# Kernel optimization log

Hardware: AMD Instinct MI355X
Metric: run time of the kernel (lower is better)

## Reference

```python
import jax, jax.numpy as jnp
import numpy as np

STRIDES = (2, 2, 2)  # from init strides
BN_EPS = 1e-3        # keras BatchNormalization default epsilon


def upsample3d(x, s):
    # x: [B, D, H, W, C] -> nearest-neighbor repeat, like keras UpSampling3D
    x = jnp.repeat(x, s[0], axis=1)
    x = jnp.repeat(x, s[1], axis=2)
    return jnp.repeat(x, s[2], axis=3)


def _conv3d_same(xi, wi):
    # xi: [D, H, W, C]; wi: [kd, kh, kw, Cin, Cout] -> SAME, stride 1
    return jax.lax.conv_general_dilated(
        xi[None], wi, window_strides=(1, 1, 1), padding='SAME',
        dimension_numbers=('NDHWC', 'DHWIO', 'NDHWC'))[0]


# per-sample dynamic conv: each batch element uses its own hypernet kernel
per_sample_conv3d = jax.vmap(_conv3d_same, in_axes=(0, 0))


def batchnorm_train(x, gamma, beta):
    # training-mode BN over N,D,H,W axes
    mean = jnp.mean(x, axis=(0, 1, 2, 3), keepdims=True)
    var = jnp.var(x, axis=(0, 1, 2, 3), keepdims=True)
    return gamma * (x - mean) * jax.lax.rsqrt(var + BN_EPS) + beta


def setup_inputs() -> dict:
    key = jax.random.key(0)
    k1, k2, k3, k4 = jax.random.split(key, 4)
    B, D, H, W, Cin, Cmid = 4, 8, 32, 32, 128, 64
    x = jax.random.normal(k1, (B, D, H, W, Cin), dtype=jnp.float32)
    # scale kernels like fan-in init to keep activations sane
    w1 = jax.random.normal(k2, (B, 3, 3, 3, Cin, Cmid), dtype=jnp.float32) * 0.02
    w2 = jax.random.normal(k3, (B, 3, 3, 3, 2 * Cmid, Cmid), dtype=jnp.float32) * 0.02
    skip = jax.random.normal(k4, (B, 2 * D, 2 * H, 2 * W, Cmid), dtype=jnp.float32)
    return {
        'x': x, 'w1': w1, 'w2': w2, 'skip': skip,
        'gamma1': jnp.ones((Cmid,), jnp.float32),
        'beta1': jnp.zeros((Cmid,), jnp.float32),
        'gamma2': jnp.ones((Cmid,), jnp.float32),
        'beta2': jnp.zeros((Cmid,), jnp.float32),
        'training': 1,
    }


def reference(x, w1, w2, skip, gamma1, beta1, gamma2, beta2, training):
    x = upsample3d(x, STRIDES)                       # [B, 2D, 2H, 2W, Cin]
    x = per_sample_conv3d(x, w1)                     # [B, 2D, 2H, 2W, Cmid]
    x = batchnorm_train(x, gamma1, beta1)
    x = jax.nn.relu(x)
    x = jnp.concatenate([x, skip], axis=-1)          # [B, 2D, 2H, 2W, 2*Cmid]
    x = per_sample_conv3d(x, w2)                     # [B, 2D, 2H, 2W, Cmid]
    x = batchnorm_train(x, gamma2, beta2)
    return jax.nn.relu(x)
```

## Files before the change

kernel.cpp:

```cpp
#include <hip/hip_runtime.h>


typedef __attribute__((ext_vector_type(8))) short short8;
typedef __attribute__((ext_vector_type(4))) float f32x4;

__device__ __forceinline__ float bf2f(unsigned short u) {
  union { unsigned int i; float f; } v; v.i = ((unsigned int)u) << 16; return v.f;
}
__device__ __forceinline__ unsigned short f2b(float f) {
  union { float ff; unsigned int u; } v; v.ff = f;
  unsigned int x = v.u;
  return (unsigned short)((x + 0x7FFFu + ((x >> 16) & 1u)) >> 16);
}
__device__ __forceinline__ unsigned int pk2(float a, float b) {
  return (unsigned int)f2b(a) | ((unsigned int)f2b(b) << 16);
}
__device__ __forceinline__ void gload16(const void* g, void* l) {
  __builtin_amdgcn_global_load_lds(
      (const __attribute__((address_space(1))) void*)g,
      (__attribute__((address_space(3))) void*)l, 16, 0, 0);
}

#define ASTR 136
#define WSTR 132

__global__ __launch_bounds__(256) void hg_wt_k(const float* __restrict__ w1,
                                               const float* __restrict__ w2,
                                               unsigned short* __restrict__ wt1,
                                               unsigned short* __restrict__ wt2) {
  __shared__ short T[64 * ASTR];
  int blk = blockIdx.x;
  int sel = blk >= 108;
  const float* w = sel ? w2 : w1;
  unsigned short* wt = sel ? wt2 : wt1;
  int bt = sel ? blk - 108 : blk;
  const float* src = w + (size_t)bt * 8192;
  int tid = threadIdx.x;
  int co = tid & 63;
  int c0 = tid >> 6;
  for (int i = 0; i < 32; ++i) {
    int ci = c0 + (i << 2);
    T[co * ASTR + ci] = (short)f2b(src[(size_t)ci * 64 + co]);
  }
  __syncthreads();
  unsigned short* dst = wt + (size_t)bt * 8192;
  for (int i = 0; i < 4; ++i) {
    int task = tid + (i << 8);
    int row = task >> 4, q = task & 15;
    *(uint4*)(dst + row * 128 + (q << 3)) = *(const uint4*)&T[row * ASTR + (q << 3)];
  }
}

__global__ __launch_bounds__(256) void hg_wc1_k(const float* __restrict__ w1,
                                                unsigned short* __restrict__ wc1) {
  __shared__ short T[64 * ASTR];
  int blk = blockIdx.x;
  int b = blk >> 6, m = blk & 63;
  int dd = m >> 4, hh = (m >> 2) & 3, ww = m & 3;
  const int ks[4] = {0, 1, 0, 2}, kc[4] = {1, 2, 2, 1};
  int tid = threadIdx.x, co = tid & 63, c0 = tid >> 6;
  const float* wb = w1 + (size_t)b * 27 * 8192;
  for (int i = 0; i < 32; ++i) {
    int ci = c0 + (i << 2);
    float s = 0.f;
    for (int a = 0; a < kc[dd]; ++a)
      for (int e = 0; e < kc[hh]; ++e)
        for (int c = 0; c < kc[ww]; ++c) {
          int tap = ((ks[dd] + a) * 3 + ks[hh] + e) * 3 + ks[ww] + c;
          s += wb[(size_t)tap * 8192 + (size_t)ci * 64 + co];
        }
    T[co * ASTR + ci] = (short)f2b(s);
  }
  __syncthreads();
  unsigned short* dst = wc1 + (size_t)blk * 8192;
  for (int i = 0; i < 4; ++i) {
    int task = tid + (i << 8);
    int row = task >> 4, q = task & 15;
    *(uint4*)(dst + row * 128 + (q << 3)) = *(const uint4*)&T[row * ASTR + (q << 3)];
  }
}

__global__ __launch_bounds__(256, 3) void hg_c1p_k(
    const unsigned short* __restrict__ xb, const unsigned short* __restrict__ wc1,
    const unsigned short* __restrict__ zb, unsigned short* __restrict__ outb,
    float* __restrict__ sums) {
  __shared__ short Xl[2 * 100 * 128];
  int tid = threadIdx.x;
  int xcd = blockIdx.x & 7, slot = blockIdx.x >> 3;
  int b = xcd & 3;
  int t = ((xcd >> 2) << 7) + slot;
  int od = t >> 4, hti = (t >> 2) & 3, wti = t & 3;
  int pd = od & 1, md = od >> 1;
  int lane = tid & 63, quad = lane >> 4, l16 = lane & 15;
  int wid = tid >> 6;
  int ph = wid >> 1, pw = wid & 1;

  for (int pl = 0; pl < 2; ++pl) {
    int sd = md + pd - 1 + pl;
    int dok = ((unsigned)sd < 8u);
    for (int i = 0; i < 7; ++i) {
      int task = tid + (i << 8);
      if (task < 1600) {
        int pos = task >> 4, pq = task & 15;
        int q = (pq & 8) | ((pq & 7) ^ (pos & 7));
        int sh = pos / 10, sw = pos - sh * 10;
        int h = (hti << 3) + sh - 1, w = (wti << 3) + sw - 1;
        const unsigned short* src = zb;
        if (dok && (unsigned)h < 32u && (unsigned)w < 32u)
          src = xb + ((((size_t)(b * 8 + sd)) * 32 + h) * 32 + w) * 128 + (q << 3);
        gload16(src, (char*)Xl + ((pl * 1600 + (i << 8) + (tid & 192)) << 4));
      }
    }
  }
  __syncthreads();

  f32x4 acc[4][4];
#pragma unroll
  for (int i = 0; i < 4; ++i)
#pragma unroll
    for (int j = 0; j < 4; ++j) acc[i][j] = (f32x4){0.f, 0.f, 0.f, 0.f};

  const unsigned short* wcb = wc1 + ((size_t)b * 64 + (pd << 5) + (ph << 3) + (pw << 1)) * 8192;

  for (int td = 0; td < 2; ++td) {
    const char* Xp = (const char*)Xl + td * 25600;
    for (int th = 0; th < 2; ++th) {
      int hb = ph + th;
      for (int tw = 0; tw < 2; ++tw) {
        int wb2 = pw + tw;
        const unsigned short* wp = wcb + (size_t)((td << 4) + (th << 2) + tw) * 8192;
#pragma unroll
        for (int ksx = 0; ksx < 4; ++ksx) {
          int cq = (ksx << 2) + quad;
          short8 av[4], bv[4];
#pragma unroll
          for (int mt = 0; mt < 4; ++mt) {
            int pos = ((mt << 1) + (l16 >> 3) + hb) * 10 + (l16 & 7) + wb2;
            int pc = (cq & 8) | ((cq & 7) ^ (pos & 7));
            av[mt] = *(const short8*)(Xp + pos * 256 + (pc << 4));
          }
#pragma unroll
          for (int nt = 0; nt < 4; ++nt)
            bv[nt] = *(const short8*)(wp + ((nt << 4) + l16) * 128 + (cq << 3));
#pragma unroll
          for (int mt = 0; mt < 4; ++mt)
#pragma unroll
            for (int nt = 0; nt < 4; ++nt)
              acc[mt][nt] = __builtin_amdgcn_mfma_f32_16x16x32_bf16(
                  av[mt], bv[nt], acc[mt][nt], 0, 0, 0);
        }
      }
    }
  }

  __syncthreads();
  float* sbf = (float*)Xl;
  int rowb = (b * 16 + od) * 64;
#pragma unroll
  for (int nt = 0; nt < 4; ++nt) {
    int n = (nt << 4) + l16;
    float s = 0.f, q2 = 0.f;
#pragma unroll
    for (int mt = 0; mt < 4; ++mt) {
      int mh = (mt << 1) + (quad >> 1);
      int oh = (((hti << 3) + mh) << 1) + ph;
      size_t rb = (size_t)(rowb + oh) * 64;
#pragma unroll
      for (int r = 0; r < 4; ++r) {
        float v = acc[mt][nt][r];
        int ow = (((wti << 3) + ((quad & 1) << 2) + r) << 1) + pw;
        outb[(rb + ow) * 64 + n] = f2b(v);
        s += v; q2 += v * v;
      }
    }
    s += __shfl_xor(s, 16); s += __shfl_xor(s, 32);
    q2 += __shfl_xor(q2, 16); q2 += __shfl_xor(q2, 32);
    if (quad == 0) { sbf[wid * 128 + n] = s; sbf[wid * 128 + 64 + n] = q2; }
  }
  __syncthreads();
  if (tid < 64) {
    float s = sbf[tid] + sbf[128 + tid] + sbf[256 + tid] + sbf[384 + tid];
    float q2 = sbf[64 + tid] + sbf[192 + tid] + sbf[320 + tid] + sbf[448 + tid];
    atomicAdd(&sums[tid], s);
    atomicAdd(&sums[64 + tid], q2);
  }
}

__global__ __launch_bounds__(256) void hg_convf_k(
    const unsigned short* __restrict__ xb, const unsigned short* __restrict__ y1n,
    const unsigned short* __restrict__ skb, const unsigned short* __restrict__ wt,
    const unsigned short* __restrict__ zb,
    unsigned short* __restrict__ outb, float* __restrict__ outf,
    float* __restrict__ sums, int mode) {
  __shared__ short Al[132 * 128];
  __shared__ short Wl[64 * 128];
  int tid = threadIdx.x;
  int xcd = blockIdx.x & 7, slot = blockIdx.x >> 3;
  int b = xcd & 3;
  int t = ((xcd >> 2) << 8) + slot;
  int m0 = (b << 16) + (t << 7);
  int od  = (t >> 5) & 15;
  int oh0 = (t << 1) & 63;
  int lane = tid & 63, quad = lane >> 4, l16 = lane & 15;
  int wm = (tid >> 6) << 5;

  f32x4 acc[2][4];
  for (int i = 0; i < 2; ++i)
    for (int j = 0; j < 4; ++j) acc[i][j] = (f32x4){0.f, 0.f, 0.f, 0.f};

  const unsigned short* wb = wt + (size_t)b * 27 * 8192;

  for (int kd = 0; kd < 3; ++kd) {
    int ud = od + kd - 1;
    int dok = ((unsigned)ud < 16u);
    for (int kh = 0; kh < 3; ++kh) {
      __syncthreads();
      for (int i = 0; i < 9; ++i) {
        int task = tid + (i << 8);
        if (task < 2112) {
          int pos = task >> 4, pq = task & 15;
          int q = (pq & 8) | ((pq & 7) ^ (pos & 7));
          int g = (pos >= 66) ? 1 : 0;
          int uw = pos - (g ? 66 : 0) - 1;
          int uh = oh0 + g + kh - 1;
          const unsigned short* src = zb;
          if (dok && (unsigned)uh < 64u && (unsigned)uw < 64u) {
            if (mode == 0) {
              src = xb + ((((size_t)(b * 8 + (ud >> 1))) * 32 + (uh >> 1)) * 32 +
                          (uw >> 1)) * 128 + (q << 3);
            } else {
              size_t srow = (((size_t)(b * 16 + ud)) * 64 + uh) * 64 + uw;
              src = (q < 8) ? (y1n + srow * 64 + (q << 3))
                            : (skb + srow * 64 + ((q - 8) << 3));
            }
          }
          gload16(src, (char*)Al + (((i << 8) + (tid & 192)) << 4));
        }
      }
      for (int kw = 0; kw < 3; ++kw) {
        if (kw) __syncthreads();
        int tap = (kd * 3 + kh) * 3 + kw;
        const unsigned short* wsrc = wb + (size_t)tap * 8192;
        {
          int co0 = tid >> 4, pq = tid & 15;
          for (int i = 0; i < 4; ++i) {
            int co = co0 + (i << 4);
            int q = (pq & 8) | ((pq & 7) ^ (co & 7));
            gload16(wsrc + co * 128 + (q << 3),
                    (char*)Wl + (((i << 8) + (tid & 192)) << 4));
          }
        }
        __syncthreads();
        for (int k0 = 0; k0 < 128; k0 += 32) {
          int cq = (k0 >> 3) + quad;
          short8 av[2], bv[4];
          for (int mt = 0; mt < 2; ++mt) {
            int r = wm + (mt << 4) + l16;
            int pos = (r >> 6) * 66 + (r & 63) + kw;
            int pc = (cq & 8) | ((cq & 7) ^ (pos & 7));
            av[mt] = *(const short8*)((const char*)Al + pos * 256 + (pc << 4));
          }
          for (int nt = 0; nt < 4; ++nt) {
            int co = (nt << 4) + l16;
            int pc = (cq & 8) | ((cq & 7) ^ (co & 7));
            bv[nt] = *(const short8*)((const char*)Wl + co * 256 + (pc << 4));
          }
          for (int mt = 0; mt < 2; ++mt)
            for (int nt = 0; nt < 4; ++nt)
              acc[mt][nt] = __builtin_amdgcn_mfma_f32_16x16x32_bf16(
                  av[mt], bv[nt], acc[mt][nt], 0, 0, 0);
        }
      }
    }
  }

  __syncthreads();
  float* sbf = (float*)Al;
  for (int nt = 0; nt < 4; ++nt) {
    int n = (nt << 4) + l16;
    float s = 0.f, q2 = 0.f;
    for (int mt = 0; mt < 2; ++mt) {
      int mbase = m0 + wm + (mt << 4) + (quad << 2);
      for (int r = 0; r < 4; ++r) {
        float v = acc[mt][nt][r];
        size_t o = (size_t)(mbase + r) * 64 + n;
        if (mode == 0) outb[o] = f2b(v);
        else outf[o] = v;
        s += v; q2 += v * v;
      }
    }
    s += __shfl_xor(s, 16); s += __shfl_xor(s, 32);
    q2 += __shfl_xor(q2, 16); q2 += __shfl_xor(q2, 32);
    if (quad == 0) { sbf[(wm >> 5) * 128 + n] = s; sbf[(wm >> 5) * 128 + 64 + n] = q2; }
  }
  __syncthreads();
  if (tid < 64) {
    float s = sbf[tid] + sbf[128 + tid] + sbf[256 + tid] + sbf[384 + tid];
    float q2 = sbf[64 + tid] + sbf[192 + tid] + sbf[320 + tid] + sbf[448 + tid];
    atomicAdd(&sums[tid], s);
    atomicAdd(&sums[64 + tid], q2);
  }
}

__global__ __launch_bounds__(256) void hg_conv_o_k(
    const float* __restrict__ xf, const unsigned short* __restrict__ y1n,
    const float* __restrict__ skip, const float* __restrict__ wf,
    const unsigned short* __restrict__ wt, const float* __restrict__ bn,
    unsigned short* __restrict__ outb, float* __restrict__ outf,
    int mode, int has_wt) {
  __shared__ short Al[132 * ASTR];
  __shared__ short Wl[64 * WSTR];
  __shared__ float sbl[128];
  int tid = threadIdx.x;
  int xcd = blockIdx.x & 7, slot = blockIdx.x >> 3;
  int b = xcd & 3;
  int t = ((xcd >> 2) << 8) + slot;
  int m0 = (b << 16) + (t << 7);
  int od  = (t >> 5) & 15;
  int oh0 = (t << 1) & 63;
  int lane = tid & 63, quad = lane >> 4, l16 = lane & 15;
  int wm = (tid >> 6) << 5;

  if (mode == 1 && tid < 128) sbl[tid] = bn[tid];

  f32x4 acc[2][4];
  for (int i = 0; i < 2; ++i)
    for (int j = 0; j < 4; ++j) acc[i][j] = (f32x4){0.f, 0.f, 0.f, 0.f};

  const float* wbf = wf + (size_t)b * 27 * 8192;
  const unsigned short* wbt = wt + (size_t)b * 27 * 8192;

  for (int kd = 0; kd < 3; ++kd) {
    int ud = od + kd - 1;
    int dok = (ud >= 0 && ud < 16);
    for (int kh = 0; kh < 3; ++kh) {
      __syncthreads();
      for (int i = 0; i < 9; ++i) {
        int task = tid + (i << 8);
        if (task < 2112) {
          int chunk = task & 15;
          int pos = task >> 4;
          int g = (pos >= 66) ? 1 : 0;
          int uwi = pos - (g ? 66 : 0);
          int uh = oh0 + g + kh - 1;
          int uw = uwi - 1;
          uint4 val = make_uint4(0u, 0u, 0u, 0u);
          if (dok && (unsigned)uh < 64u && (unsigned)uw < 64u) {
            if (mode == 0) {
              size_t src = ((((size_t)(b * 8 + (ud >> 1))) * 32 + (uh >> 1)) * 32 +
                            (uw >> 1)) * 128 + (chunk << 3);
              float4 f0 = *(const float4*)(xf + src);
              float4 f1 = *(const float4*)(xf + src + 4);
              val.x = pk2(f0.x, f0.y); val.y = pk2(f0.z, f0.w);
              val.z = pk2(f1.x, f1.y); val.w = pk2(f1.z, f1.w);
            } else {
              size_t srow = (((size_t)(b * 16 + ud)) * 64 + uh) * 64 + uw;
              if (chunk < 8) {
                uint4 raw = *(const uint4*)(y1n + srow * 64 + (chunk << 3));
                unsigned int u[4] = {raw.x, raw.y, raw.z, raw.w};
                unsigned int o[4];
                int c0 = chunk << 3;
                for (int q = 0; q < 4; ++q) {
                  int c = c0 + q * 2;
                  float f0 = sbl[c] * bf2f((unsigned short)(u[q] & 0xFFFFu)) + sbl[64 + c];
                  float f1 = sbl[c + 1] * bf2f((unsigned short)(u[q] >> 16)) + sbl[64 + c + 1];
                  o[q] = pk2(f0 > 0.f ? f0 : 0.f, f1 > 0.f ? f1 : 0.f);
                }
                val = make_uint4(o[0], o[1], o[2], o[3]);
              } else {
                const float* sp = skip + srow * 64 + ((chunk - 8) << 3);
                float4 f0 = *(const float4*)(sp);
                float4 f1 = *(const float4*)(sp + 4);
                val.x = pk2(f0.x, f0.y); val.y = pk2(f0.z, f0.w);
                val.z = pk2(f1.x, f1.y); val.w = pk2(f1.z, f1.w);
              }
            }
          }
          *(uint4*)&Al[pos * ASTR + (chunk << 3)] = val;
        }
      }
      for (int kw = 0; kw < 3; ++kw) {
        if (kw) __syncthreads();
        int tap = (kd * 3 + kh) * 3 + kw;
        if (has_wt) {
          const unsigned short* wsrc = wbt + (size_t)tap * 8192;
          for (int i = 0; i < 4; ++i) {
            int task = tid + (i << 8);
            int co = task >> 4, q = task & 15;
            *(uint4*)&Wl[co * WSTR + (q << 3)] = *(const uint4*)(wsrc + co * 128 + (q << 3));
          }
        } else {
          const float* wp = wbf + (size_t)tap * 8192 + (tid & 63);
          int wco = tid & 63;
          int ci0 = (tid >> 6) << 5;
          for (int c = 0; c < 32; c += 2) {
            float f0 = wp[(size_t)(ci0 + c) * 64];
            float f1 = wp[(size_t)(ci0 + c + 1) * 64];
            *(unsigned int*)&Wl[wco * WSTR + ci0 + c] = pk2(f0, f1);
          }
        }
        __syncthreads();
        for (int k0 = 0; k0 < 128; k0 += 32) {
          int kk = k0 + (quad << 3);
          union { uint4 u; short8 s; } cv;
          short8 av[2];
          for (int mt = 0; mt < 2; ++mt) {
            int r = wm + (mt << 4) + l16;
            int g = r >> 6, ow = r & 63;
            cv.u = *(const uint4*)&Al[(g * 66 + ow + kw) * ASTR + kk];
            av[mt] = cv.s;
          }
          short8 bv[4];
          for (int nt = 0; nt < 4; ++nt) {
            int base = ((nt << 4) + l16) * WSTR + kk;
            uint2 lo = *(const uint2*)&Wl[base];
            uint2 hi = *(const uint2*)&Wl[base + 4];
            cv.u = make_uint4(lo.x, lo.y, hi.x, hi.y);
            bv[nt] = cv.s;
          }
          for (int mt = 0; mt < 2; ++mt)
            for (int nt = 0; nt < 4; ++nt)
              acc[mt][nt] = __builtin_amdgcn_mfma_f32_16x16x32_bf16(
                  av[mt], bv[nt], acc[mt][nt], 0, 0, 0);
        }
      }
    }
  }

  for (int mt = 0; mt < 2; ++mt) {
    int mbase = m0 + wm + (mt << 4) + (quad << 2);
    for (int nt = 0; nt < 4; ++nt) {
      int n = (nt << 4) + l16;
      for (int r = 0; r < 4; ++r) {
        float v = acc[mt][nt][r];
        size_t o = (size_t)(mbase + r) * 64 + n;
        if (mode == 0) outb[o] = f2b(v);
        else outf[o] = v;
      }
    }
  }
}

__global__ void hg_zero_k(float* __restrict__ p, int n) {
  for (int i = threadIdx.x; i < n; i += 256) p[i] = 0.f;
}

__global__ __launch_bounds__(256) void hg_stats_k(const unsigned short* __restrict__ yb,
                                                  const float* __restrict__ yf, int isf,
                                                  float* __restrict__ sums) {
  int t = threadIdx.x;
  int c = t & 63;
  int r0 = blockIdx.x * 4 + (t >> 6);
  float sum = 0.f, ss = 0.f;
  for (int r = r0; r < 262144; r += 4096) {
    size_t idx = (size_t)r * 64 + c;
    float v = isf ? yf[idx] : bf2f(yb[idx]);
    sum += v; ss += v * v;
  }
  atomicAdd(&sums[c], sum);
  atomicAdd(&sums[64 + c], ss);
}

__global__ void hg_fin_k(float* __restrict__ sb, const float* __restrict__ gm,
                         const float* __restrict__ bt) {
  int c = threadIdx.x;
  float invN = 1.f / 262144.f;
  float mean = sb[c] * invN;
  float var  = sb[64 + c] * invN - mean * mean;
  float sc = gm[c] * rsqrtf(var + 1e-3f);
  sb[c] = sc;
  sb[64 + c] = bt[c] - mean * sc;
}

__global__ __launch_bounds__(256) void hg_cvt_k(const float* __restrict__ s,
                                                unsigned short* __restrict__ d) {
  size_t i = ((size_t)blockIdx.x * 256 + threadIdx.x) << 3;
  float4 a = *(const float4*)(s + i);
  float4 c = *(const float4*)(s + i + 4);
  uint4 o;
  o.x = pk2(a.x, a.y); o.y = pk2(a.z, a.w);
  o.z = pk2(c.x, c.y); o.w = pk2(c.z, c.w);
  *(uint4*)(d + i) = o;
}

__global__ __launch_bounds__(256) void hg_bnb_k(unsigned short* __restrict__ y,
                                                const float* __restrict__ sb) {
  size_t i = ((size_t)blockIdx.x * 256 + threadIdx.x) << 3;
  int c0 = (int)(i & 63);
  uint4 v = *(uint4*)(y + i);
  unsigned int u[4] = {v.x, v.y, v.z, v.w};
  for (int q = 0; q < 4; ++q) {
    int c = c0 + q * 2;
    float f0 = sb[c] * bf2f((unsigned short)(u[q] & 0xFFFFu)) + sb[64 + c];
    float f1 = sb[c + 1] * bf2f((unsigned short)(u[q] >> 16)) + sb[64 + c + 1];
    u[q] = pk2(f0 > 0.f ? f0 : 0.f, f1 > 0.f ? f1 : 0.f);
  }
  *(uint4*)(y + i) = make_uint4(u[0], u[1], u[2], u[3]);
}

__global__ __launch_bounds__(256) void hg_bnrelu_f_k(float* __restrict__ y,
                                                     const float* __restrict__ sb) {
  size_t i = (size_t)blockIdx.x * 256 + threadIdx.x;
  int c4 = ((int)i & 15) << 2;
  float4 v = *(float4*)(y + i * 4);
  float f;
  f = sb[c4]     * v.x + sb[64 + c4];     v.x = f > 0.f ? f : 0.f;
  f = sb[c4 + 1] * v.y + sb[64 + c4 + 1]; v.y = f > 0.f ? f : 0.f;
  f = sb[c4 + 2] * v.z + sb[64 + c4 + 2]; v.z = f > 0.f ? f : 0.f;
  f = sb[c4 + 3] * v.w + sb[64 + c4 + 3]; v.w = f > 0.f ? f : 0.f;
  *(float4*)(y + i * 4) = v;
}

extern "C" void kernel_launch(void* const* d_in, const int* in_sizes, int n_in,
                              void* d_out, int out_size, void* d_ws, size_t ws_size,
                              hipStream_t stream) {
  (void)out_size;
  int ix = 0, iw1 = 1, iw2 = 2, isk = 3, ig1 = 4, ib1 = 5, ig2 = 6, ib2 = 7;
  if (n_in >= 9 && in_sizes[0] == 4194304 && in_sizes[1] == 884736 &&
      in_sizes[3] == 16777216 && in_sizes[4] == 64) {
  } else if (n_in >= 9 && in_sizes[0] == 64 && in_sizes[4] == 16777216 &&
             in_sizes[6] == 884736 && in_sizes[8] == 4194304) {
    ib1 = 0; ib2 = 1; ig1 = 2; ig2 = 3; isk = 4; iw1 = 6; iw2 = 7; ix = 8;
  } else {
    return;
  }
  if (ws_size < (32ull << 20) + 2048ull) return;

  const float* x    = (const float*)d_in[ix];
  const float* w1   = (const float*)d_in[iw1];
  const float* w2   = (const float*)d_in[iw2];
  const float* skip = (const float*)d_in[isk];
  const float* g1   = (const float*)d_in[ig1];
  const float* b1   = (const float*)d_in[ib1];
  const float* g2   = (const float*)d_in[ig2];
  const float* b2   = (const float*)d_in[ib2];
  float* out = (float*)d_out;

  const size_t OFF_SUMS = 32ull << 20;
  const size_t OFF_ZB   = OFF_SUMS + 2048;
  const size_t OFF_WT1  = OFF_ZB + 256;
  const size_t OFF_WT2  = OFF_WT1 + 1769472;
  const size_t OFF_XB   = OFF_WT2 + 1769472;
  const size_t OFF_SKB  = OFF_XB + 8388608;
  const size_t OFF_WC1  = OFF_SKB + 33554432;
  const size_t NEED     = OFF_WC1 + 4194304;

  unsigned short* y1 = (unsigned short*)d_ws;
  float* sums  = (float*)((char*)d_ws + OFF_SUMS);
  float* sums1 = sums;
  float* sums2 = sums + 128;

  if (ws_size >= NEED) {
    unsigned short* zb  = (unsigned short*)((char*)d_ws + OFF_ZB);
    unsigned short* wt1 = (unsigned short*)((char*)d_ws + OFF_WT1);
    unsigned short* wt2 = (unsigned short*)((char*)d_ws + OFF_WT2);
    unsigned short* xb  = (unsigned short*)((char*)d_ws + OFF_XB);
    unsigned short* skb = (unsigned short*)((char*)d_ws + OFF_SKB);
    unsigned short* wc1 = (unsigned short*)((char*)d_ws + OFF_WC1);

    hg_zero_k<<<1, 256, 0, stream>>>(sums, 576);
    hg_wt_k<<<216, 256, 0, stream>>>(w1, w2, wt1, wt2);
    hg_wc1_k<<<256, 256, 0, stream>>>(w1, wc1);
    hg_cvt_k<<<2048, 256, 0, stream>>>(x, xb);
    hg_cvt_k<<<8192, 256, 0, stream>>>(skip, skb);
    hg_c1p_k<<<1024, 256, 0, stream>>>(xb, wc1, zb, y1, sums1);
    hg_fin_k<<<1, 64, 0, stream>>>(sums1, g1, b1);
    hg_bnb_k<<<8192, 256, 0, stream>>>(y1, sums1);
    hg_convf_k<<<2048, 256, 0, stream>>>(xb, y1, skb, wt2, zb, y1, out, sums2, 1);
    hg_fin_k<<<1, 64, 0, stream>>>(sums2, g2, b2);
    hg_bnrelu_f_k<<<16384, 256, 0, stream>>>(out, sums2);
  } else {
    unsigned short* wt1 = (unsigned short*)((char*)d_ws + (32ull << 20) + 2048ull);
    unsigned short* wt2 = wt1 + 884736ull;
    const size_t WS_NEED = (32ull << 20) + 2048ull + 2ull * 884736ull * 2ull;
    int has_wt = (ws_size >= WS_NEED) ? 1 : 0;

    hg_zero_k<<<1, 256, 0, stream>>>(sums, 512);
    if (has_wt) hg_wt_k<<<216, 256, 0, stream>>>(w1, w2, wt1, wt2);
    hg_conv_o_k<<<2048, 256, 0, stream>>>(x, y1, skip, w1, wt1, sums1, y1, out, 0, has_wt);
    hg_stats_k<<<1024, 256, 0, stream>>>(y1, out, 0, sums1);
    hg_fin_k<<<1, 64, 0, stream>>>(sums1, g1, b1);
    hg_conv_o_k<<<2048, 256, 0, stream>>>(x, y1, skip, w2, wt2, sums1, y1, out, 1, has_wt);
    hg_stats_k<<<1024, 256, 0, stream>>>(y1, out, 1, sums2);
    hg_fin_k<<<1, 64, 0, stream>>>(sums2, g2, b2);
    hg_bnrelu_f_k<<<16384, 256, 0, stream>>>(out, sums2);
  }
}
```

Before: 462.6 us.

## Retile second conv into 128-thread 4x32 blocks and spread BN stat atomics

Replaces the generic second-conv kernel with a dedicated one. Each 128-thread block covers a 4-row by 32-column output tile and each wave holds a 4x4 MFMA accumulator set, which raises MFMA work per LDS weight load and reduces halo overhead per block. BatchNorm sum and sum-of-squares atomics are now split across 8 slots chosen by XCD, and a new finalize kernel adds them back together, to cut atomic contention on the same addresses. The risks are fewer waves per block, which may hurt latency hiding, and more registers per thread.

```diff
diff --git a/kernel.cpp b/kernel.cpp
--- a/kernel.cpp
+++ b/kernel.cpp
@@ -181,31 +181,31 @@
   if (tid < 64) {
     float s = sbf[tid] + sbf[128 + tid] + sbf[256 + tid] + sbf[384 + tid];
     float q2 = sbf[64 + tid] + sbf[192 + tid] + sbf[320 + tid] + sbf[448 + tid];
-    atomicAdd(&sums[tid], s);
-    atomicAdd(&sums[64 + tid], q2);
-  }
-}
-
-__global__ __launch_bounds__(256) void hg_convf_k(
-    const unsigned short* __restrict__ xb, const unsigned short* __restrict__ y1n,
-    const unsigned short* __restrict__ skb, const unsigned short* __restrict__ wt,
-    const unsigned short* __restrict__ zb,
-    unsigned short* __restrict__ outb, float* __restrict__ outf,
-    float* __restrict__ sums, int mode) {
-  __shared__ short Al[132 * 128];
+    int sl = (blockIdx.x & 7) << 7;
+    atomicAdd(&sums[sl + tid], s);
+    atomicAdd(&sums[sl + 64 + tid], q2);
+  }
+}
+
+__global__ __launch_bounds__(128) void hg_c2_k(
+    const unsigned short* __restrict__ y1n, const unsigned short* __restrict__ skb,
+    const unsigned short* __restrict__ wt, const unsigned short* __restrict__ zb,
+    float* __restrict__ outf, float* __restrict__ sums) {
+  __shared__ short Al[136 * 128];
   __shared__ short Wl[64 * 128];
   int tid = threadIdx.x;
   int xcd = blockIdx.x & 7, slot = blockIdx.x >> 3;
   int b = xcd & 3;
   int t = ((xcd >> 2) << 8) + slot;
-  int m0 = (b << 16) + (t << 7);
-  int od  = (t >> 5) & 15;
-  int oh0 = (t << 1) & 63;
+  int od = t >> 5, ohg = (t >> 1) & 15, owg = t & 1;
+  int oh0 = ohg << 2, ow0 = owg << 5;
   int lane = tid & 63, quad = lane >> 4, l16 = lane & 15;
-  int wm = (tid >> 6) << 5;
-
-  f32x4 acc[2][4];
-  for (int i = 0; i < 2; ++i)
+  int wid = tid >> 6;
+
+  f32x4 acc[4][4];
+#pragma unroll
+  for (int i = 0; i < 4; ++i)
+#pragma unroll
     for (int j = 0; j < 4; ++j) acc[i][j] = (f32x4){0.f, 0.f, 0.f, 0.f};
 
   const unsigned short* wb = wt + (size_t)b * 27 * 8192;
@@ -215,57 +215,54 @@
     int dok = ((unsigned)ud < 16u);
     for (int kh = 0; kh < 3; ++kh) {
       __syncthreads();
-      for (int i = 0; i < 9; ++i) {
-        int task = tid + (i << 8);
-        if (task < 2112) {
-          int pos = task >> 4, pq = task & 15;
-          int q = (pq & 8) | ((pq & 7) ^ (pos & 7));
-          int g = (pos >= 66) ? 1 : 0;
-          int uw = pos - (g ? 66 : 0) - 1;
-          int uh = oh0 + g + kh - 1;
-          const unsigned short* src = zb;
-          if (dok && (unsigned)uh < 64u && (unsigned)uw < 64u) {
-            if (mode == 0) {
-              src = xb + ((((size_t)(b * 8 + (ud >> 1))) * 32 + (uh >> 1)) * 32 +
-                          (uw >> 1)) * 128 + (q << 3);
-            } else {
-              size_t srow = (((size_t)(b * 16 + ud)) * 64 + uh) * 64 + uw;
-              src = (q < 8) ? (y1n + srow * 64 + (q << 3))
-                            : (skb + srow * 64 + ((q - 8) << 3));
-            }
-          }
-          gload16(src, (char*)Al + (((i << 8) + (tid & 192)) << 4));
-        }
+      for (int i = 0; i < 17; ++i) {
+        int task = tid + (i << 7);
+        int pos = task >> 4, pq = task & 15;
+        int q = (pq & 8) | ((pq & 7) ^ (pos & 7));
+        int g = pos / 34;
+        int uwi = pos - g * 34;
+        int uh = oh0 + g + kh - 1;
+        int uw = ow0 + uwi - 1;
+        const unsigned short* src = zb;
+        if (dok && (unsigned)uh < 64u && (unsigned)uw < 64u) {
+          size_t srow = (((size_t)(b * 16 + ud)) * 64 + uh) * 64 + uw;
+          src = (q < 8) ? (y1n + srow * 64 + (q << 3))
+                        : (skb + srow * 64 + ((q - 8) << 3));
+        }
+        gload16(src, (char*)Al + (((i << 7) + (tid & 64)) << 4));
       }
       for (int kw = 0; kw < 3; ++kw) {
         if (kw) __syncthreads();
         int tap = (kd * 3 + kh) * 3 + kw;
         const unsigned short* wsrc = wb + (size_t)tap * 8192;
-        {
-          int co0 = tid >> 4, pq = tid & 15;
-          for (int i = 0; i < 4; ++i) {
-            int co = co0 + (i << 4);
-            int q = (pq & 8) | ((pq & 7) ^ (co & 7));
-            gload16(wsrc + co * 128 + (q << 3),
-                    (char*)Wl + (((i << 8) + (tid & 192)) << 4));
-          }
+        for (int i = 0; i < 8; ++i) {
+          int task = tid + (i << 7);
+          int co = task >> 4, pq = task & 15;
+          int q = (pq & 8) | ((pq & 7) ^ (co & 7));
+          gload16(wsrc + co * 128 + (q << 3),
+                  (char*)Wl + (((i << 7) + (tid & 64)) << 4));
         }
         __syncthreads();
-        for (int k0 = 0; k0 < 128; k0 += 32) {
-          int cq = (k0 >> 3) + quad;
-          short8 av[2], bv[4];
-          for (int mt = 0; mt < 2; ++mt) {
-            int r = wm + (mt << 4) + l16;
-            int pos = (r >> 6) * 66 + (r & 63) + kw;
+#pragma unroll
+        for (int k0 = 0; k0 < 4; ++k0) {
+          int cq = (k0 << 2) + quad;
+          short8 av[4], bv[4];
+#pragma unroll
+          for (int mt = 0; mt < 4; ++mt) {
+            int mg = (wid << 2) + mt;
+            int pos = (mg >> 1) * 34 + ((mg & 1) << 4) + l16 + kw;
             int pc = (cq & 8) | ((cq & 7) ^ (pos & 7));
             av[mt] = *(const short8*)((const char*)Al + pos * 256 + (pc << 4));
           }
+#pragma unroll
           for (int nt = 0; nt < 4; ++nt) {
             int co = (nt << 4) + l16;
             int pc = (cq & 8) | ((cq & 7) ^ (co & 7));
             bv[nt] = *(const short8*)((const char*)Wl + co * 256 + (pc << 4));
           }
-          for (int mt = 0; mt < 2; ++mt)
+#pragma unroll
+          for (int mt = 0; mt < 4; ++mt)
+#pragma unroll
             for (int nt = 0; nt < 4; ++nt)
               acc[mt][nt] = __builtin_amdgcn_mfma_f32_16x16x32_bf16(
                   av[mt], bv[nt], acc[mt][nt], 0, 0, 0);
@@ -276,29 +273,35 @@
 
   __syncthreads();
   float* sbf = (float*)Al;
+  int rowb = (b * 16 + od) * 64;
+#pragma unroll
   for (int nt = 0; nt < 4; ++nt) {
     int n = (nt << 4) + l16;
     float s = 0.f, q2 = 0.f;
-    for (int mt = 0; mt < 2; ++mt) {
-      int mbase = m0 + wm + (mt << 4) + (quad << 2);
+#pragma unroll
+    for (int mt = 0; mt < 4; ++mt) {
+      int mg = (wid << 2) + mt;
+      int oh = oh0 + (mg >> 1);
+      int owb = ow0 + ((mg & 1) << 4) + (quad << 2);
+      size_t rb = ((size_t)(rowb + oh) * 64 + owb) * 64 + n;
+#pragma unroll
       for (int r = 0; r < 4; ++r) {
         float v = acc[mt][nt][r];
-        size_t o = (size_t)(mbase + r) * 64 + n;
-        if (mode == 0) outb[o] = f2b(v);
-        else outf[o] = v;
+        outf[rb + (size_t)r * 64] = v;
         s += v; q2 += v * v;
       }
     }
     s += __shfl_xor(s, 16); s += __shfl_xor(s, 32);
     q2 += __shfl_xor(q2, 16); q2 += __shfl_xor(q2, 32);
-    if (quad == 0) { sbf[(wm >> 5) * 128 + n] = s; sbf[(wm >> 5) * 128 + 64 + n] = q2; }
+    if (quad == 0) { sbf[wid * 128 + n] = s; sbf[wid * 128 + 64 + n] = q2; }
   }
   __syncthreads();
   if (tid < 64) {
-    float s = sbf[tid] + sbf[128 + tid] + sbf[256 + tid] + sbf[384 + tid];
-    float q2 = sbf[64 + tid] + sbf[192 + tid] + sbf[320 + tid] + sbf[448 + tid];
-    atomicAdd(&sums[tid], s);
-    atomicAdd(&sums[64 + tid], q2);
+    float s = sbf[tid] + sbf[128 + tid];
+    float q2 = sbf[64 + tid] + sbf[192 + tid];
+    int sl = (blockIdx.x & 7) << 7;
+    atomicAdd(&sums[sl + tid], s);
+    atomicAdd(&sums[sl + 64 + tid], q2);
   }
 }
 
@@ -472,6 +475,19 @@
   sb[64 + c] = bt[c] - mean * sc;
 }
 
+__global__ void hg_fin8_k(float* __restrict__ sb, const float* __restrict__ gm,
+                          const float* __restrict__ bt) {
+  int c = threadIdx.x;
+  float s = 0.f, q2 = 0.f;
+  for (int k = 0; k < 8; ++k) { s += sb[(k << 7) + c]; q2 += sb[(k << 7) + 64 + c]; }
+  float invN = 1.f / 262144.f;
+  float mean = s * invN;
+  float var  = q2 * invN - mean * mean;
+  float sc = gm[c] * rsqrtf(var + 1e-3f);
+  sb[c] = sc;
+  sb[64 + c] = bt[c] - mean * sc;
+}
+
 __global__ __launch_bounds__(256) void hg_cvt_k(const float* __restrict__ s,
                                                 unsigned short* __restrict__ d) {
   size_t i = ((size_t)blockIdx.x * 256 + threadIdx.x) << 3;
@@ -537,7 +553,7 @@
   float* out = (float*)d_out;
 
   const size_t OFF_SUMS = 32ull << 20;
-  const size_t OFF_ZB   = OFF_SUMS + 2048;
+  const size_t OFF_ZB   = OFF_SUMS + 8192;
   const size_t OFF_WT1  = OFF_ZB + 256;
   const size_t OFF_WT2  = OFF_WT1 + 1769472;
   const size_t OFF_XB   = OFF_WT2 + 1769472;
@@ -546,11 +562,11 @@
   const size_t NEED     = OFF_WC1 + 4194304;
 
   unsigned short* y1 = (unsigned short*)d_ws;
-  float* sums  = (float*)((char*)d_ws + OFF_SUMS);
-  float* sums1 = sums;
-  float* sums2 = sums + 128;
 
   if (ws_size >= NEED) {
+    float* sums  = (float*)((char*)d_ws + OFF_SUMS);
+    float* sums1 = sums;
+    float* sums2 = sums + 1024;
     unsigned short* zb  = (unsigned short*)((char*)d_ws + OFF_ZB);
     unsigned short* wt1 = (unsigned short*)((char*)d_ws + OFF_WT1);
     unsigned short* wt2 = (unsigned short*)((char*)d_ws + OFF_WT2);
@@ -558,18 +574,21 @@
     unsigned short* skb = (unsigned short*)((char*)d_ws + OFF_SKB);
     unsigned short* wc1 = (unsigned short*)((char*)d_ws + OFF_WC1);
 
-    hg_zero_k<<<1, 256, 0, stream>>>(sums, 576);
+    hg_zero_k<<<1, 256, 0, stream>>>(sums, 2112);
     hg_wt_k<<<216, 256, 0, stream>>>(w1, w2, wt1, wt2);
     hg_wc1_k<<<256, 256, 0, stream>>>(w1, wc1);
     hg_cvt_k<<<2048, 256, 0, stream>>>(x, xb);
     hg_cvt_k<<<8192, 256, 0, stream>>>(skip, skb);
     hg_c1p_k<<<1024, 256, 0, stream>>>(xb, wc1, zb, y1, sums1);
-    hg_fin_k<<<1, 64, 0, stream>>>(sums1, g1, b1);
+    hg_fin8_k<<<1, 64, 0, stream>>>(sums1, g1, b1);
     hg_bnb_k<<<8192, 256, 0, stream>>>(y1, sums1);
-    hg_convf_k<<<2048, 256, 0, stream>>>(xb, y1, skb, wt2, zb, y1, out, sums2, 1);
-    hg_fin_k<<<1, 64, 0, stream>>>(sums2, g2, b2);
+    hg_c2_k<<<2048, 128, 0, stream>>>(y1, skb, wt2, zb, out, sums2);
+    hg_fin8_k<<<1, 64, 0, stream>>>(sums2, g2, b2);
     hg_bnrelu_f_k<<<16384, 256, 0, stream>>>(out, sums2);
   } else {
+    float* sums  = (float*)((char*)d_ws + (32ull << 20));
+    float* sums1 = sums;
+    float* sums2 = sums + 128;
     unsigned short* wt1 = (unsigned short*)((char*)d_ws + (32ull << 20) + 2048ull);
     unsigned short* wt2 = wt1 + 884736ull;
     const size_t WS_NEED = (32ull << 20) + 2048ull + 2ull * 884736ull * 2ull;
```

After: 488.7 us. 5.6% more time.

## Read conv2 weights directly from global in fragment layout and shard BN stat atomics

Applied to the files above, without the earlier changes.

Adds a weight pre-pass that stores conv2 weights in an MFMA-fragment-friendly layout, so the conv2 kernel reads B operands straight from global/L2 instead of staging each tap through LDS. This removes the per-tap LDS weight copy and two barriers per tap, and adds a launch bound that asks for higher occupancy. BN statistic atomics are spread across 8 slots keyed by block index, and a new finalize kernel sums the slots, to cut atomic contention. The cost is more global/L2 traffic for weight fragments that are re-read by every wave.

```diff
diff --git a/kernel.cpp b/kernel.cpp
--- a/kernel.cpp
+++ b/kernel.cpp
@@ -48,6 +48,27 @@
     int task = tid + (i << 8);
     int row = task >> 4, q = task & 15;
     *(uint4*)(dst + row * 128 + (q << 3)) = *(const uint4*)&T[row * ASTR + (q << 3)];
+  }
+}
+
+__global__ __launch_bounds__(256) void hg_wtg_k(const float* __restrict__ w2,
+                                                unsigned short* __restrict__ wtg) {
+  __shared__ short T[64 * ASTR];
+  int bt = blockIdx.x;
+  const float* src = w2 + (size_t)bt * 8192;
+  int tid = threadIdx.x;
+  int co = tid & 63;
+  int c0 = tid >> 6;
+  for (int i = 0; i < 32; ++i) {
+    int ci = c0 + (i << 2);
+    T[co * ASTR + ci] = (short)f2b(src[(size_t)ci * 64 + co]);
+  }
+  __syncthreads();
+  unsigned short* dst = wtg + (size_t)bt * 8192;
+  for (int i = 0; i < 4; ++i) {
+    int task = tid + (i << 8);
+    int row = task >> 4, q = task & 15;
+    *(uint4*)(dst + ((q << 6) + row) * 8) = *(const uint4*)&T[row * ASTR + (q << 3)];
   }
 }
 
@@ -181,19 +202,17 @@
   if (tid < 64) {
     float s = sbf[tid] + sbf[128 + tid] + sbf[256 + tid] + sbf[384 + tid];
     float q2 = sbf[64 + tid] + sbf[192 + tid] + sbf[320 + tid] + sbf[448 + tid];
-    atomicAdd(&sums[tid], s);
-    atomicAdd(&sums[64 + tid], q2);
-  }
-}
-
-__global__ __launch_bounds__(256) void hg_convf_k(
-    const unsigned short* __restrict__ xb, const unsigned short* __restrict__ y1n,
-    const unsigned short* __restrict__ skb, const unsigned short* __restrict__ wt,
-    const unsigned short* __restrict__ zb,
-    unsigned short* __restrict__ outb, float* __restrict__ outf,
-    float* __restrict__ sums, int mode) {
+    int sl = (blockIdx.x & 7) << 7;
+    atomicAdd(&sums[sl + tid], s);
+    atomicAdd(&sums[sl + 64 + tid], q2);
+  }
+}
+
+__global__ __launch_bounds__(256, 4) void hg_c2g_k(
+    const unsigned short* __restrict__ y1n, const unsigned short* __restrict__ skb,
+    const unsigned short* __restrict__ wtg, const unsigned short* __restrict__ zb,
+    float* __restrict__ outf, float* __restrict__ sums) {
   __shared__ short Al[132 * 128];
-  __shared__ short Wl[64 * 128];
   int tid = threadIdx.x;
   int xcd = blockIdx.x & 7, slot = blockIdx.x >> 3;
   int b = xcd & 3;
@@ -208,7 +227,7 @@
   for (int i = 0; i < 2; ++i)
     for (int j = 0; j < 4; ++j) acc[i][j] = (f32x4){0.f, 0.f, 0.f, 0.f};
 
-  const unsigned short* wb = wt + (size_t)b * 27 * 8192;
+  const unsigned short* wb = wtg + (size_t)b * 27 * 8192;
 
   for (int kd = 0; kd < 3; ++kd) {
     int ud = od + kd - 1;
@@ -225,47 +244,34 @@
           int uh = oh0 + g + kh - 1;
           const unsigned short* src = zb;
           if (dok && (unsigned)uh < 64u && (unsigned)uw < 64u) {
-            if (mode == 0) {
-              src = xb + ((((size_t)(b * 8 + (ud >> 1))) * 32 + (uh >> 1)) * 32 +
-                          (uw >> 1)) * 128 + (q << 3);
-            } else {
-              size_t srow = (((size_t)(b * 16 + ud)) * 64 + uh) * 64 + uw;
-              src = (q < 8) ? (y1n + srow * 64 + (q << 3))
-                            : (skb + srow * 64 + ((q - 8) << 3));
-            }
+            size_t srow = (((size_t)(b * 16 + ud)) * 64 + uh) * 64 + uw;
+            src = (q < 8) ? (y1n + srow * 64 + (q << 3))
+                          : (skb + srow * 64 + ((q - 8) << 3));
           }
           gload16(src, (char*)Al + (((i << 8) + (tid & 192)) << 4));
         }
       }
+      __syncthreads();
+#pragma clang loop unroll(disable)
       for (int kw = 0; kw < 3; ++kw) {
-        if (kw) __syncthreads();
-        int tap = (kd * 3 + kh) * 3 + kw;
-        const unsigned short* wsrc = wb + (size_t)tap * 8192;
-        {
-          int co0 = tid >> 4, pq = tid & 15;
-          for (int i = 0; i < 4; ++i) {
-            int co = co0 + (i << 4);
-            int q = (pq & 8) | ((pq & 7) ^ (co & 7));
-            gload16(wsrc + co * 128 + (q << 3),
-                    (char*)Wl + (((i << 8) + (tid & 192)) << 4));
-          }
-        }
-        __syncthreads();
-        for (int k0 = 0; k0 < 128; k0 += 32) {
-          int cq = (k0 >> 3) + quad;
+        const unsigned short* wp = wb + (size_t)((kd * 3 + kh) * 3 + kw) * 8192;
+#pragma unroll
+        for (int k0 = 0; k0 < 4; ++k0) {
+          int cq = (k0 << 2) + quad;
           short8 av[2], bv[4];
+#pragma unroll
           for (int mt = 0; mt < 2; ++mt) {
             int r = wm + (mt << 4) + l16;
             int pos = (r >> 6) * 66 + (r & 63) + kw;
             int pc = (cq & 8) | ((cq & 7) ^ (pos & 7));
             av[mt] = *(const short8*)((const char*)Al + pos * 256 + (pc << 4));
           }
-          for (int nt = 0; nt < 4; ++nt) {
-            int co = (nt << 4) + l16;
-            int pc = (cq & 8) | ((cq & 7) ^ (co & 7));
-            bv[nt] = *(const short8*)((const char*)Wl + co * 256 + (pc << 4));
-          }
+#pragma unroll
+          for (int nt = 0; nt < 4; ++nt)
+            bv[nt] = *(const short8*)(wp + (((cq << 6) + (nt << 4) + l16) << 3));
+#pragma unroll
           for (int mt = 0; mt < 2; ++mt)
+#pragma unroll
             for (int nt = 0; nt < 4; ++nt)
               acc[mt][nt] = __builtin_amdgcn_mfma_f32_16x16x32_bf16(
                   av[mt], bv[nt], acc[mt][nt], 0, 0, 0);
@@ -283,9 +289,7 @@
       int mbase = m0 + wm + (mt << 4) + (quad << 2);
       for (int r = 0; r < 4; ++r) {
         float v = acc[mt][nt][r];
-        size_t o = (size_t)(mbase + r) * 64 + n;
-        if (mode == 0) outb[o] = f2b(v);
-        else outf[o] = v;
+        outf[(size_t)(mbase + r) * 64 + n] = v;
         s += v; q2 += v * v;
       }
     }
@@ -297,8 +301,9 @@
   if (tid < 64) {
     float s = sbf[tid] + sbf[128 + tid] + sbf[256 + tid] + sbf[384 + tid];
     float q2 = sbf[64 + tid] + sbf[192 + tid] + sbf[320 + tid] + sbf[448 + tid];
-    atomicAdd(&sums[tid], s);
-    atomicAdd(&sums[64 + tid], q2);
+    int sl = (blockIdx.x & 7) << 7;
+    atomicAdd(&sums[sl + tid], s);
+    atomicAdd(&sums[sl + 64 + tid], q2);
   }
 }
 
@@ -472,6 +477,19 @@
   sb[64 + c] = bt[c] - mean * sc;
 }
 
+__global__ void hg_fin8_k(float* __restrict__ sb, const float* __restrict__ gm,
+                          const float* __restrict__ bt) {
+  int c = threadIdx.x;
+  float s = 0.f, q2 = 0.f;
+  for (int k = 0; k < 8; ++k) { s += sb[(k << 7) + c]; q2 += sb[(k << 7) + 64 + c]; }
+  float invN = 1.f / 262144.f;
+  float mean = s * invN;
+  float var  = q2 * invN - mean * mean;
+  float sc = gm[c] * rsqrtf(var + 1e-3f);
+  sb[c] = sc;
+  sb[64 + c] = bt[c] - mean * sc;
+}
+
 __global__ __launch_bounds__(256) void hg_cvt_k(const float* __restrict__ s,
                                                 unsigned short* __restrict__ d) {
   size_t i = ((size_t)blockIdx.x * 256 + threadIdx.x) << 3;
@@ -537,7 +555,7 @@
   float* out = (float*)d_out;
 
   const size_t OFF_SUMS = 32ull << 20;
-  const size_t OFF_ZB   = OFF_SUMS + 2048;
+  const size_t OFF_ZB   = OFF_SUMS + 8192;
   const size_t OFF_WT1  = OFF_ZB + 256;
   const size_t OFF_WT2  = OFF_WT1 + 1769472;
   const size_t OFF_XB   = OFF_WT2 + 1769472;
@@ -546,30 +564,32 @@
   const size_t NEED     = OFF_WC1 + 4194304;
 
   unsigned short* y1 = (unsigned short*)d_ws;
-  float* sums  = (float*)((char*)d_ws + OFF_SUMS);
-  float* sums1 = sums;
-  float* sums2 = sums + 128;
 
   if (ws_size >= NEED) {
+    float* sums  = (float*)((char*)d_ws + OFF_SUMS);
+    float* sums1 = sums;
+    float* sums2 = sums + 1024;
     unsigned short* zb  = (unsigned short*)((char*)d_ws + OFF_ZB);
-    unsigned short* wt1 = (unsigned short*)((char*)d_ws + OFF_WT1);
-    unsigned short* wt2 = (unsigned short*)((char*)d_ws + OFF_WT2);
+    unsigned short* wtg = (unsigned short*)((char*)d_ws + OFF_WT1);
     unsigned short* xb  = (unsigned short*)((char*)d_ws + OFF_XB);
     unsigned short* skb = (unsigned short*)((char*)d_ws + OFF_SKB);
     unsigned short* wc1 = (unsigned short*)((char*)d_ws + OFF_WC1);
 
-    hg_zero_k<<<1, 256, 0, stream>>>(sums, 576);
-    hg_wt_k<<<216, 256, 0, stream>>>(w1, w2, wt1, wt2);
+    hg_zero_k<<<1, 256, 0, stream>>>(sums, 2112);
+    hg_wtg_k<<<108, 256, 0, stream>>>(w2, wtg);
     hg_wc1_k<<<256, 256, 0, stream>>>(w1, wc1);
     hg_cvt_k<<<2048, 256, 0, stream>>>(x, xb);
     hg_cvt_k<<<8192, 256, 0, stream>>>(skip, skb);
     hg_c1p_k<<<1024, 256, 0, stream>>>(xb, wc1, zb, y1, sums1);
-    hg_fin_k<<<1, 64, 0, stream>>>(sums1, g1, b1);
+    hg_fin8_k<<<1, 64, 0, stream>>>(sums1, g1, b1);
     hg_bnb_k<<<8192, 256, 0, stream>>>(y1, sums1);
-    hg_convf_k<<<2048, 256, 0, stream>>>(xb, y1, skb, wt2, zb, y1, out, sums2, 1);
-    hg_fin_k<<<1, 64, 0, stream>>>(sums2, g2, b2);
+    hg_c2g_k<<<2048, 256, 0, stream>>>(y1, skb, wtg, zb, out, sums2);
+    hg_fin8_k<<<1, 64, 0, stream>>>(sums2, g2, b2);
     hg_bnrelu_f_k<<<16384, 256, 0, stream>>>(out, sums2);
   } else {
+    float* sums  = (float*)((char*)d_ws + (32ull << 20));
+    float* sums1 = sums;
+    float* sums2 = sums + 128;
     unsigned short* wt1 = (unsigned short*)((char*)d_ws + (32ull << 20) + 2048ull);
     unsigned short* wt2 = wt1 + 884736ull;
     const size_t WS_NEED = (32ull << 20) + 2048ull + 2ull * 884736ull * 2ull;
```

Measured after the change: 524.5 us. 1.13x slower.
